# Optimization experiments

Hardware: AMD Instinct MI355X
Metric: run time of the kernel (lower is better)

Reference implementation:

```python
import jax, jax.numpy as jnp
import numpy as np

D_M, L_OBS, ALPHA, D_H = 1024, 2048, 8192, 2048


def setup_inputs() -> dict:
    key = jax.random.key(0)
    k1, k2, k3, k4, k5 = jax.random.split(key, 5)
    x_ts = jax.random.normal(k1, (D_M, L_OBS), dtype=jnp.float32)
    t_ts = jax.random.randint(k2, (D_M, L_OBS), 0, ALPHA, dtype=jnp.int32)
    global_means = jax.random.normal(k3, (D_M,), dtype=jnp.float32)
    W = jax.random.normal(k4, (D_H, D_M), dtype=jnp.float32) * 0.02
    b = jax.random.normal(k5, (D_H,), dtype=jnp.float32) * 0.02
    return {"x_ts": x_ts, "t_ts": t_ts, "global_means": global_means, "W": W, "b": b}


def reference(x_ts, t_ts, global_means, W, b):
    d_m, l_obs = x_ts.shape
    alpha = ALPHA
    # valid observations: non-NaN value and time index within [0, alpha)
    valid = (~jnp.isnan(x_ts)) & (t_ts >= 0) & (t_ts < alpha)
    # route invalid observations to a dummy column `alpha` (dropped afterwards)
    idx = jnp.where(valid, t_ts, alpha)                      # [d_m, l_obs]
    rows = jnp.arange(d_m)[:, None]
    xs = jnp.where(valid, x_ts, 0.0)
    grid_val = jnp.zeros((d_m, alpha + 1), x_ts.dtype).at[rows, idx].set(xs)[:, :alpha]
    grid_ok = jnp.zeros((d_m, alpha + 1), bool).at[rows, idx].set(valid)[:, :alpha]
    # forward-fill: last valid index via cummax, init with global mean
    pos = jnp.arange(alpha)[None, :]                         # [1, alpha]
    last = jax.lax.cummax(jnp.where(grid_ok, pos, -1), axis=1)  # [d_m, alpha]
    filled = jnp.take_along_axis(grid_val, jnp.maximum(last, 0), axis=1)
    regular = jnp.where(last >= 0, filled, global_means[:, None])  # [d_m, alpha]
    # 1x1 conv over time == GEMM over feature dim; output [alpha, d_h]
    return jnp.einsum('ma,hm->ah', regular, W) + b[None, :]
```

## Files before the change

kernel.cpp:

```cpp
#include <hip/hip_runtime.h>
#include <stdint.h>

#define D_M   1024
#define L_OBS 2048
#define ALPHA 8192
#define D_H   2048

typedef __attribute__((ext_vector_type(8))) short short8;
typedef __attribute__((ext_vector_type(4))) float f32x4;

__device__ inline unsigned short f2bf(float f) {
  union { float f; unsigned u; } c; c.f = f;
  unsigned u = c.u;
  u += 0x7fffu + ((u >> 16) & 1u);
  return (unsigned short)(u >> 16);
}

__global__ __launch_bounds__(1024) void impute_fill(
    const float* __restrict__ x_ts, const int* __restrict__ t_ts,
    const float* __restrict__ gmean, unsigned short* __restrict__ dst,
    int transposed_out) {
  __shared__ unsigned long long pack[ALPHA];
  __shared__ float s_wv[16];
  __shared__ int   s_wh[16];

  const int m    = blockIdx.x;
  const int tid  = threadIdx.x;
  const int lane = tid & 63;
  const int wv   = tid >> 6;

  #pragma unroll
  for (int i = 0; i < 8; ++i) pack[tid + i * 1024] = 0ull;
  __syncthreads();

  #pragma unroll
  for (int j = 0; j < 2; ++j) {
    const int l = tid + j * 1024;
    const float xv = x_ts[(size_t)m * L_OBS + l];
    const int   tv = t_ts[(size_t)m * L_OBS + l];
    if ((xv == xv) && (tv >= 0) && (tv < ALPHA)) {
      union { float f; unsigned u; } c; c.f = xv;
      atomicMax(&pack[tv], ((unsigned long long)(l + 1) << 32) | c.u);
    }
  }
  __syncthreads();

  const int base = tid * 8;
  int has = 0; float lv = 0.f;
  #pragma unroll
  for (int i = 0; i < 8; ++i) {
    const unsigned long long p = pack[base + i];
    if (p >> 32) { has = 1; lv = __uint_as_float((unsigned)p); }
  }

  int ihas = has; float ilv = lv;
  #pragma unroll
  for (int d = 1; d < 64; d <<= 1) {
    const float pv = __shfl_up(ilv, d, 64);
    const int   ph = __shfl_up(ihas, d, 64);
    if (lane >= d && !ihas) { ihas = ph; ilv = pv; }
  }
  if (lane == 63) { s_wh[wv] = ihas; s_wv[wv] = ilv; }
  __syncthreads();
  if (wv == 0 && lane < 16) {
    int h2 = s_wh[lane]; float v2 = s_wv[lane];
    #pragma unroll
    for (int d = 1; d < 16; d <<= 1) {
      const float pv = __shfl_up(v2, d, 16);
      const int   ph = __shfl_up(h2, d, 16);
      if (lane >= d && !h2) { h2 = ph; v2 = pv; }
    }
    s_wh[lane] = h2; s_wv[lane] = v2;
  }
  __syncthreads();

  const float xlv = __shfl_up(ilv, 1, 64);
  const int   xh_ = __shfl_up(ihas, 1, 64);
  const int   xhas = (lane > 0) ? xh_ : 0;
  float running;
  if (xhas)                         running = xlv;
  else if (wv > 0 && s_wh[wv - 1])  running = s_wv[wv - 1];
  else                              running = gmean[m];

  if (transposed_out) {
    #pragma unroll
    for (int i = 0; i < 8; ++i) {
      const unsigned long long p = pack[base + i];
      if (p >> 32) running = __uint_as_float((unsigned)p);
      dst[(size_t)(base + i) * D_M + m] = f2bf(running);
    }
  } else {
    short8 ov;
    #pragma unroll
    for (int i = 0; i < 8; ++i) {
      const unsigned long long p = pack[base + i];
      if (p >> 32) running = __uint_as_float((unsigned)p);
      ov[i] = (short)f2bf(running);
    }
    *(short8*)&dst[(size_t)m * ALPHA + base] = ov;
  }
}

__global__ __launch_bounds__(256) void transpose_bf(
    const unsigned short* __restrict__ reg, unsigned short* __restrict__ regT) {
  __shared__ unsigned short tile[64 * 64];
  const int t  = threadIdx.x;
  const int m0 = (blockIdx.x & 15) * 64;
  const int A0 = (blockIdx.x >> 4) * 64;

  #pragma unroll
  for (int i = 0; i < 2; ++i) {
    const int m  = i * 32 + (t >> 3);
    const int ao = (t & 7) * 8;
    short8 v = *(const short8*)&reg[(size_t)(m0 + m) * ALPHA + A0 + ao];
    const int s = ((m & 7) ^ (m >> 3)) << 3;
    *(short8*)&tile[m * 64 + (ao ^ s)] = v;
  }
  __syncthreads();
  #pragma unroll
  for (int i = 0; i < 2; ++i) {
    const int a  = i * 32 + (t >> 3);
    const int mo = (t & 7) * 8;
    short8 ov;
    #pragma unroll
    for (int j = 0; j < 8; ++j) {
      const int mm = mo + j;
      const int s  = ((mm & 7) ^ (mm >> 3)) << 3;
      ov[j] = (short)tile[mm * 64 + (a ^ s)];
    }
    *(short8*)&regT[(size_t)(A0 + a) * D_M + m0 + mo] = ov;
  }
}

__global__ __launch_bounds__(256) void wconv(const float* __restrict__ W,
                                             unsigned short* __restrict__ Wb) {
  const int i = (blockIdx.x * 256 + threadIdx.x) * 4;
  const float4 w = *reinterpret_cast<const float4*>(&W[i]);
  ushort4 o;
  o.x = f2bf(w.x); o.y = f2bf(w.y); o.z = f2bf(w.z); o.w = f2bf(w.w);
  *reinterpret_cast<ushort4*>(&Wb[i]) = o;
}

#define GNT3 32

__device__ inline void gload_lds16(const void* g, void* l) {
  __builtin_amdgcn_global_load_lds(
      (const __attribute__((address_space(1))) unsigned int*)g,
      (__attribute__((address_space(3))) unsigned int*)l, 16, 0, 0);
}

#define BARX() { asm volatile("" ::: "memory"); __builtin_amdgcn_s_barrier(); \
                 asm volatile("" ::: "memory"); }
#define LGKM0() asm volatile("s_waitcnt lgkmcnt(0)" ::: "memory")
#define SB0()   __builtin_amdgcn_sched_barrier(0)

__global__ __launch_bounds__(512, 4) void gemm_bias(
    const unsigned short* __restrict__ A,
    const unsigned short* __restrict__ B,
    const float* __restrict__ bias, float* __restrict__ out) {
  __shared__ char lds[73728];

  const int tid  = threadIdx.x;
  const int lane = tid & 63;
  const int wid  = tid >> 6;
  const int wm   = wid >> 2;
  const int wn   = wid & 3;
  const int xcd  = blockIdx.x & 7;
  const int pos  = blockIdx.x >> 3;
  const int bm   = xcd * 8 + (pos >> 3);
  const int bn   = pos & 7;
  const int a0r = bm * 128, h0 = bn * 256;

  f32x4 acc[4][4] = {};
  short8 af[4], bf[4];

  const int r0 = tid >> 2, s0 = tid & 3;
  const int swzB = (s0 ^ ((r0 >> 1) & 3)) * 16;
  const char* Asrc  = (const char*)A + ((size_t)(a0r + r0) * D_M) * 2 + swzB;
  const char* Bsrc0 = (const char*)B + ((size_t)(h0 + r0) * D_M) * 2 + swzB;
  const char* Bsrc1 = Bsrc0 + (size_t)128 * D_M * 2;

#define STAGE(S, kt) { \
  gload_lds16(Asrc  + (size_t)(kt) * 64, lds + (S) * 8192 + tid * 16); \
  char* bd_ = lds + 24576 + (S) * 16384 + tid * 16; \
  gload_lds16(Bsrc0 + (size_t)(kt) * 64, bd_); \
  gload_lds16(Bsrc1 + (size_t)(kt) * 64, bd_ + 8192); }

  const int rl  = lane & 15;
  const int rsw = (((lane >> 4) ^ ((rl >> 1) & 3))) * 16;
  const int Aro = (wm * 64 + rl) * 64 + rsw;
  const int Bro = 24576 + (wn * 64 + rl) * 64 + rsw;

#define TILE(S, SST, T) { \
  _Pragma("unroll") \
  for (int mf = 0; mf < 4; ++mf) \
    af[mf] = *(const short8*)(lds + (S) * 8192 + Aro + mf * 1024); \
  _Pragma("unroll") \
  for (int nf = 0; nf < 4; ++nf) \
    bf[nf] = *(const short8*)(lds + (S) * 16384 + Bro + nf * 1024); \
  if ((T) < GNT3 - 2) STAGE(SST, (T) + 2); \
  LGKM0(); SB0(); \
  __builtin_amdgcn_s_setprio(1); \
  _Pragma("unroll") \
  for (int mf = 0; mf < 4; ++mf) \
    _Pragma("unroll") \
    for (int nf = 0; nf < 4; ++nf) \
      acc[mf][nf] = __builtin_amdgcn_mfma_f32_16x16x32_bf16(af[mf], bf[nf], acc[mf][nf], 0, 0, 0); \
  __builtin_amdgcn_s_setprio(0); \
  if ((T) < GNT3 - 2)       { asm volatile("s_waitcnt vmcnt(3)" ::: "memory"); } \
  else if ((T) == GNT3 - 2) { asm volatile("s_waitcnt vmcnt(0)" ::: "memory"); } \
  if ((T) < GNT3 - 1) BARX(); }

  STAGE(0, 0); STAGE(1, 1);
  asm volatile("s_waitcnt vmcnt(3)" ::: "memory");
  BARX();

  for (int tt = 0; tt < GNT3 - 2; tt += 3) {
    TILE(0, 2, tt);
    TILE(1, 0, tt + 1);
    TILE(2, 1, tt + 2);
  }
  TILE(0, 2, 30);
  TILE(1, 0, 31);

  const int cl = lane & 15, rq = lane >> 4;
  #pragma unroll
  for (int nf = 0; nf < 4; ++nf) {
    const int h = h0 + wn * 64 + nf * 16 + cl;
    const float bv = bias[h];
    #pragma unroll
    for (int mf = 0; mf < 4; ++mf) {
      const int ar = a0r + wm * 64 + mf * 16 + rq * 4;
      #pragma unroll
      for (int r = 0; r < 4; ++r)
        out[(size_t)(ar + r) * D_H + h] = acc[mf][nf][r] + bv;
    }
  }
#undef STAGE
#undef TILE
}

extern "C" void kernel_launch(void* const* d_in, const int* in_sizes, int n_in,
                              void* d_out, int out_size, void* d_ws, size_t ws_size,
                              hipStream_t stream) {
  const float* x  = (const float*)d_in[0];
  const int*   t  = (const int*)d_in[1];
  const float* gm = (const float*)d_in[2];
  const float* W  = (const float*)d_in[3];
  const float* b  = (const float*)d_in[4];
  float* out = (float*)d_out;

  const size_t SZ_REG = (size_t)ALPHA * D_M * 2;
  const size_t SZ_WB  = (size_t)D_H * D_M * 2;
  const int GRID = (ALPHA / 128) * (D_H / 256);

  if (ws_size >= 2 * SZ_REG + SZ_WB) {
    unsigned short* reg  = (unsigned short*)d_ws;
    unsigned short* regT = (unsigned short*)((char*)d_ws + SZ_REG);
    unsigned short* Wb   = (unsigned short*)((char*)d_ws + 2 * SZ_REG);
    impute_fill<<<D_M, 1024, 0, stream>>>(x, t, gm, reg, 0);
    wconv<<<(D_H * D_M) / 1024, 256, 0, stream>>>(W, Wb);
    transpose_bf<<<(ALPHA / 64) * (D_M / 64), 256, 0, stream>>>(reg, regT);
    gemm_bias<<<GRID, 512, 0, stream>>>(regT, Wb, b, out);
  } else {
    unsigned short* regT = (unsigned short*)d_ws;
    unsigned short* Wb   = (unsigned short*)((char*)d_ws + SZ_REG);
    impute_fill<<<D_M, 1024, 0, stream>>>(x, t, gm, regT, 1);
    wconv<<<(D_H * D_M) / 1024, 256, 0, stream>>>(W, Wb);
    gemm_bias<<<GRID, 512, 0, stream>>>(regT, Wb, b, out);
  }
}
```

Measured before the change: 66.51 us.

## Pack scatter grid into 32-bit LDS words and fuse W conversion with transpose

The scatter grid in LDS shrinks from 64-bit to 32-bit entries by storing a 16-bit observation index alongside the bf16 value. This halves shared memory and allows 512-thread blocks that each process 16 grid cells. The separate weight conversion kernel is merged into the transpose kernel through extra blocks, which removes one launch. Rounding to bf16 happens before the fill rather than after, which gives the same values, and l+1 still fits in 16 bits.

```diff
diff --git a/kernel.cpp b/kernel.cpp
--- a/kernel.cpp
+++ b/kernel.cpp
@@ -16,13 +16,13 @@
   return (unsigned short)(u >> 16);
 }
 
-__global__ __launch_bounds__(1024) void impute_fill(
+__global__ __launch_bounds__(512) void impute_fill(
     const float* __restrict__ x_ts, const int* __restrict__ t_ts,
     const float* __restrict__ gmean, unsigned short* __restrict__ dst,
     int transposed_out) {
-  __shared__ unsigned long long pack[ALPHA];
-  __shared__ float s_wv[16];
-  __shared__ int   s_wh[16];
+  __shared__ unsigned pack[ALPHA];
+  __shared__ float s_wv[8];
+  __shared__ int   s_wh[8];
 
   const int m    = blockIdx.x;
   const int tid  = threadIdx.x;
@@ -30,27 +30,26 @@
   const int wv   = tid >> 6;
 
   #pragma unroll
-  for (int i = 0; i < 8; ++i) pack[tid + i * 1024] = 0ull;
-  __syncthreads();
-
-  #pragma unroll
-  for (int j = 0; j < 2; ++j) {
-    const int l = tid + j * 1024;
+  for (int i = 0; i < 4; ++i)
+    *reinterpret_cast<uint4*>(&pack[tid * 16 + i * 4]) = make_uint4(0u, 0u, 0u, 0u);
+  __syncthreads();
+
+  #pragma unroll
+  for (int j = 0; j < 4; ++j) {
+    const int l = tid + j * 512;
     const float xv = x_ts[(size_t)m * L_OBS + l];
     const int   tv = t_ts[(size_t)m * L_OBS + l];
-    if ((xv == xv) && (tv >= 0) && (tv < ALPHA)) {
-      union { float f; unsigned u; } c; c.f = xv;
-      atomicMax(&pack[tv], ((unsigned long long)(l + 1) << 32) | c.u);
-    }
-  }
-  __syncthreads();
-
-  const int base = tid * 8;
+    if ((xv == xv) && (tv >= 0) && (tv < ALPHA))
+      atomicMax(&pack[tv], ((unsigned)(l + 1) << 16) | (unsigned)f2bf(xv));
+  }
+  __syncthreads();
+
+  const int base = tid * 16;
   int has = 0; float lv = 0.f;
   #pragma unroll
-  for (int i = 0; i < 8; ++i) {
-    const unsigned long long p = pack[base + i];
-    if (p >> 32) { has = 1; lv = __uint_as_float((unsigned)p); }
+  for (int i = 0; i < 16; ++i) {
+    const unsigned p = pack[base + i];
+    if (p >> 16) { has = 1; lv = __uint_as_float(p << 16); }
   }
 
   int ihas = has; float ilv = lv;
@@ -62,12 +61,12 @@
   }
   if (lane == 63) { s_wh[wv] = ihas; s_wv[wv] = ilv; }
   __syncthreads();
-  if (wv == 0 && lane < 16) {
+  if (wv == 0 && lane < 8) {
     int h2 = s_wh[lane]; float v2 = s_wv[lane];
     #pragma unroll
-    for (int d = 1; d < 16; d <<= 1) {
-      const float pv = __shfl_up(v2, d, 16);
-      const int   ph = __shfl_up(h2, d, 16);
+    for (int d = 1; d < 8; d <<= 1) {
+      const float pv = __shfl_up(v2, d, 8);
+      const int   ph = __shfl_up(h2, d, 8);
       if (lane >= d && !h2) { h2 = ph; v2 = pv; }
     }
     s_wh[lane] = h2; s_wv[lane] = v2;
@@ -84,27 +83,45 @@
 
   if (transposed_out) {
     #pragma unroll
+    for (int i = 0; i < 16; ++i) {
+      const unsigned p = pack[base + i];
+      if (p >> 16) running = __uint_as_float(p << 16);
+      dst[(size_t)(base + i) * D_M + m] = f2bf(running);
+    }
+  } else {
+    short8 ov0, ov1;
+    #pragma unroll
     for (int i = 0; i < 8; ++i) {
-      const unsigned long long p = pack[base + i];
-      if (p >> 32) running = __uint_as_float((unsigned)p);
-      dst[(size_t)(base + i) * D_M + m] = f2bf(running);
-    }
-  } else {
-    short8 ov;
-    #pragma unroll
-    for (int i = 0; i < 8; ++i) {
-      const unsigned long long p = pack[base + i];
-      if (p >> 32) running = __uint_as_float((unsigned)p);
-      ov[i] = (short)f2bf(running);
-    }
-    *(short8*)&dst[(size_t)m * ALPHA + base] = ov;
-  }
-}
-
-__global__ __launch_bounds__(256) void transpose_bf(
-    const unsigned short* __restrict__ reg, unsigned short* __restrict__ regT) {
+      const unsigned p = pack[base + i];
+      if (p >> 16) running = __uint_as_float(p << 16);
+      ov0[i] = (short)f2bf(running);
+    }
+    #pragma unroll
+    for (int i = 8; i < 16; ++i) {
+      const unsigned p = pack[base + i];
+      if (p >> 16) running = __uint_as_float(p << 16);
+      ov1[i - 8] = (short)f2bf(running);
+    }
+    *(short8*)&dst[(size_t)m * ALPHA + base]     = ov0;
+    *(short8*)&dst[(size_t)m * ALPHA + base + 8] = ov1;
+  }
+}
+
+__global__ __launch_bounds__(256) void prep(
+    const unsigned short* __restrict__ reg, unsigned short* __restrict__ regT,
+    const float* __restrict__ W, unsigned short* __restrict__ Wb) {
   __shared__ unsigned short tile[64 * 64];
-  const int t  = threadIdx.x;
+  const int t = threadIdx.x;
+
+  if (blockIdx.x >= 2048) {
+    const int i = ((blockIdx.x - 2048) * 256 + t) * 4;
+    const float4 w = *reinterpret_cast<const float4*>(&W[i]);
+    ushort4 o;
+    o.x = f2bf(w.x); o.y = f2bf(w.y); o.z = f2bf(w.z); o.w = f2bf(w.w);
+    *reinterpret_cast<ushort4*>(&Wb[i]) = o;
+    return;
+  }
+
   const int m0 = (blockIdx.x & 15) * 64;
   const int A0 = (blockIdx.x >> 4) * 64;
 
@@ -258,14 +275,13 @@
     unsigned short* reg  = (unsigned short*)d_ws;
     unsigned short* regT = (unsigned short*)((char*)d_ws + SZ_REG);
     unsigned short* Wb   = (unsigned short*)((char*)d_ws + 2 * SZ_REG);
-    impute_fill<<<D_M, 1024, 0, stream>>>(x, t, gm, reg, 0);
-    wconv<<<(D_H * D_M) / 1024, 256, 0, stream>>>(W, Wb);
-    transpose_bf<<<(ALPHA / 64) * (D_M / 64), 256, 0, stream>>>(reg, regT);
+    impute_fill<<<D_M, 512, 0, stream>>>(x, t, gm, reg, 0);
+    prep<<<4096, 256, 0, stream>>>(reg, regT, W, Wb);
     gemm_bias<<<GRID, 512, 0, stream>>>(regT, Wb, b, out);
   } else {
     unsigned short* regT = (unsigned short*)d_ws;
     unsigned short* Wb   = (unsigned short*)((char*)d_ws + SZ_REG);
-    impute_fill<<<D_M, 1024, 0, stream>>>(x, t, gm, regT, 1);
+    impute_fill<<<D_M, 512, 0, stream>>>(x, t, gm, regT, 1);
     wconv<<<(D_H * D_M) / 1024, 256, 0, stream>>>(W, Wb);
     gemm_bias<<<GRID, 512, 0, stream>>>(regT, Wb, b, out);
   }
```

Measured after the change: 61.23 us. 7.9% less time.
